# Optimization experiments

Measured on AMD Instinct MI355X. Metric: run time of the kernel, lower is better.

## Reference

```python
import jax, jax.numpy as jnp
import numpy as np
from jax.scipy.special import logsumexp

B, C, K = 4096, 8192, 8  # batch, num_classes, positives per sample


def setup_inputs() -> dict:
    key = jax.random.key(0)
    predictions = jax.random.normal(key, (B, C), dtype=jnp.float32)
    # Distinct positive class indices per row (mimics np.setdiff1d assume_unique=True):
    # pairwise diffs within a row are nonzero multiples of 997 with |diff| < C, so distinct mod C.
    labels = (jnp.arange(B, dtype=jnp.int32)[:, None] * 131
              + jnp.arange(K, dtype=jnp.int32)[None, :] * 997) % C
    return {"predictions": predictions, "labels": labels}


def reference(predictions, labels):
    # For each sample b and each positive p in labels[b], the original computes
    # CrossEntropy over the class subset {p} U negatives(b) with target index 0:
    #   term = -pred[b,p] + logsumexp(pred[b,p], pred[b, negatives(b)])
    # Negatives are shared across all positives of a sample, so compute their
    # logsumexp once per row and combine with each positive via logaddexp.
    Bn, Cn = predictions.shape
    rows = jnp.arange(Bn)[:, None]                                   # [B,1]
    pos_mask = jnp.zeros((Bn, Cn), dtype=bool).at[rows, labels].set(True)  # [B,C]
    lse_neg = logsumexp(predictions, axis=-1, where=~pos_mask)       # [B]
    pos_logits = jnp.take_along_axis(predictions, labels, axis=1)    # [B,K]
    loss_terms = jnp.logaddexp(pos_logits, lse_neg[:, None]) - pos_logits  # [B,K]
    # sum over all (sample, positive) pairs, divided by their count
    return jnp.sum(loss_terms) / loss_terms.size
```

## Files before the change

### kernel.cpp

```cpp
#include <hip/hip_runtime.h>


constexpr int B = 4096;
constexpr int C = 8192;
constexpr int K = 8;
constexpr int BLOCK = 256;
constexpr int VEC_PER_THREAD = C / 4 / BLOCK;

__global__ __launch_bounds__(BLOCK)
void mlsm_row_kernel(const float* __restrict__ pred,
                     const int* __restrict__ labels,
                     float* __restrict__ out) {
    const int b   = blockIdx.x;
    const int tid = threadIdx.x;
    const float* row = pred + (size_t)b * C;
    const float4* row4 = reinterpret_cast<const float4*>(row);

    float s = 0.0f;
#pragma unroll
    for (int i = 0; i < VEC_PER_THREAD; ++i) {
        float4 v = row4[tid + i * BLOCK];
        s += __expf(v.x) + __expf(v.y) + __expf(v.z) + __expf(v.w);
    }

#pragma unroll
    for (int off = 32; off > 0; off >>= 1)
        s += __shfl_down(s, off, 64);

    __shared__ float wave_sum[BLOCK / 64];
    const int wave = tid >> 6;
    if ((tid & 63) == 0) wave_sum[wave] = s;
    __syncthreads();

    if (tid == 0) {
        float total = wave_sum[0] + wave_sum[1] + wave_sum[2] + wave_sum[3];

        const int* lab = labels + b * K;
        float pos[K];
        float epos[K];
        float sum_pos = 0.0f;
#pragma unroll
        for (int k = 0; k < K; ++k) {
            pos[k]  = row[lab[k]];
            epos[k] = __expf(pos[k]);
            sum_pos += epos[k];
        }
        const float sum_neg = total - sum_pos;

        float loss = 0.0f;
#pragma unroll
        for (int k = 0; k < K; ++k)
            loss += __logf(epos[k] + sum_neg) - pos[k];

        atomicAdd(out, loss * (1.0f / (float)(B * K)));
    }
}

extern "C" void kernel_launch(void* const* d_in, const int* in_sizes, int n_in,
                              void* d_out, int out_size, void* d_ws, size_t ws_size,
                              hipStream_t stream) {
    const float* pred  = (const float*)d_in[0];
    const int* labels  = (const int*)d_in[1];
    float* out         = (float*)d_out;

    hipMemsetAsync(out, 0, sizeof(float), stream);

    mlsm_row_kernel<<<B, BLOCK, 0, stream>>>(pred, labels, out);
}
```

Measured before the change: 208.0 us.

## Replace global atomic with per-row partials and a separate reduction kernel

Each row block now writes its loss to a workspace array instead of doing a single-address atomicAdd. A second one-block kernel sums those partials, which removes the memset. The row kernel also issues all of its float4 loads before the exponentials, keeps four independent accumulators, and spreads the 8 positive-label terms across 8 lanes using xor shuffles. The cost is an extra kernel launch and a workspace buffer. The loss now depends on d_ws being large enough for B floats.

```diff
diff --git a/kernel.cpp b/kernel.cpp
--- a/kernel.cpp
+++ b/kernel.cpp
@@ -5,65 +5,96 @@
 constexpr int C = 8192;
 constexpr int K = 8;
 constexpr int BLOCK = 256;
-constexpr int VEC_PER_THREAD = C / 4 / BLOCK;
+constexpr int VPT = C / 4 / BLOCK;
 
 __global__ __launch_bounds__(BLOCK)
 void mlsm_row_kernel(const float* __restrict__ pred,
                      const int* __restrict__ labels,
-                     float* __restrict__ out) {
+                     float* __restrict__ partial) {
     const int b   = blockIdx.x;
     const int tid = threadIdx.x;
     const float* row = pred + (size_t)b * C;
     const float4* row4 = reinterpret_cast<const float4*>(row);
 
-    float s = 0.0f;
+    float4 v[VPT];
 #pragma unroll
-    for (int i = 0; i < VEC_PER_THREAD; ++i) {
-        float4 v = row4[tid + i * BLOCK];
-        s += __expf(v.x) + __expf(v.y) + __expf(v.z) + __expf(v.w);
+    for (int i = 0; i < VPT; ++i)
+        v[i] = row4[tid + i * BLOCK];
+
+    float s0 = 0.f, s1 = 0.f, s2 = 0.f, s3 = 0.f;
+#pragma unroll
+    for (int i = 0; i < VPT; ++i) {
+        s0 += __expf(v[i].x);
+        s1 += __expf(v[i].y);
+        s2 += __expf(v[i].z);
+        s3 += __expf(v[i].w);
     }
+    float s = (s0 + s1) + (s2 + s3);
 
 #pragma unroll
     for (int off = 32; off > 0; off >>= 1)
         s += __shfl_down(s, off, 64);
 
     __shared__ float wave_sum[BLOCK / 64];
-    const int wave = tid >> 6;
-    if ((tid & 63) == 0) wave_sum[wave] = s;
+    if ((tid & 63) == 0) wave_sum[tid >> 6] = s;
     __syncthreads();
 
-    if (tid == 0) {
-        float total = wave_sum[0] + wave_sum[1] + wave_sum[2] + wave_sum[3];
+    if (tid < K) {
+        const float total =
+            (wave_sum[0] + wave_sum[1]) + (wave_sum[2] + wave_sum[3]);
 
-        const int* lab = labels + b * K;
-        float pos[K];
-        float epos[K];
-        float sum_pos = 0.0f;
+        const int cls = labels[b * K + tid];
+        const float p = row[cls];
+        const float e = __expf(p);
+
+        float sum_pos = e;
 #pragma unroll
-        for (int k = 0; k < K; ++k) {
-            pos[k]  = row[lab[k]];
-            epos[k] = __expf(pos[k]);
-            sum_pos += epos[k];
-        }
+        for (int m = 1; m < K; m <<= 1)
+            sum_pos += __shfl_xor(sum_pos, m, K);
+
         const float sum_neg = total - sum_pos;
+        float term = __logf(e + sum_neg) - p;
+#pragma unroll
+        for (int m = 1; m < K; m <<= 1)
+            term += __shfl_xor(term, m, K);
 
-        float loss = 0.0f;
+        if (tid == 0) partial[b] = term;
+    }
+}
+
+__global__ __launch_bounds__(BLOCK)
+void mlsm_reduce_kernel(const float* __restrict__ partial,
+                        float* __restrict__ out) {
+    const int tid = threadIdx.x;
+    const float4* p4 = reinterpret_cast<const float4*>(partial);
+
+    float s = 0.f;
 #pragma unroll
-        for (int k = 0; k < K; ++k)
-            loss += __logf(epos[k] + sum_neg) - pos[k];
+    for (int i = 0; i < B / 4 / BLOCK; ++i) {
+        float4 v = p4[tid + i * BLOCK];
+        s += (v.x + v.y) + (v.z + v.w);
+    }
+#pragma unroll
+    for (int off = 32; off > 0; off >>= 1)
+        s += __shfl_down(s, off, 64);
 
-        atomicAdd(out, loss * (1.0f / (float)(B * K)));
-    }
+    __shared__ float wave_sum[BLOCK / 64];
+    if ((tid & 63) == 0) wave_sum[tid >> 6] = s;
+    __syncthreads();
+
+    if (tid == 0)
+        out[0] = ((wave_sum[0] + wave_sum[1]) + (wave_sum[2] + wave_sum[3]))
+                 * (1.0f / (float)(B * K));
 }
 
 extern "C" void kernel_launch(void* const* d_in, const int* in_sizes, int n_in,
                               void* d_out, int out_size, void* d_ws, size_t ws_size,
                               hipStream_t stream) {
-    const float* pred  = (const float*)d_in[0];
-    const int* labels  = (const int*)d_in[1];
-    float* out         = (float*)d_out;
+    const float* pred = (const float*)d_in[0];
+    const int* labels = (const int*)d_in[1];
+    float* out        = (float*)d_out;
+    float* partial    = (float*)d_ws;
 
-    hipMemsetAsync(out, 0, sizeof(float), stream);
-
-    mlsm_row_kernel<<<B, BLOCK, 0, stream>>>(pred, labels, out);
+    mlsm_row_kernel<<<B, BLOCK, 0, stream>>>(pred, labels, partial);
+    mlsm_reduce_kernel<<<1, BLOCK, 0, stream>>>(partial, out);
 }
```

Result: faster. 187.2 us (-10.0%).
